# Kernel tuning notes

Hardware: AMD Instinct MI355X
Metric: run time of the kernel (lower is better)

## Reference

```python
import jax, jax.numpy as jnp
import numpy as np

N, L, D, H = 2, 2048, 1024, 16
DK = D // H  # 64


def setup_inputs() -> dict:
    key = jax.random.key(0)
    ks = jax.random.split(key, 8)
    Xq = jax.random.normal(ks[0], (N, L, D), dtype=jnp.float32)
    Xk = jax.random.normal(ks[1], (N, L, D), dtype=jnp.float32)
    Xv = jax.random.normal(ks[2], (N, L, D), dtype=jnp.float32)
    mask_2d = jax.random.randint(ks[3], (N, L, L), 0, 2, dtype=jnp.int32)
    scale = 0.02
    Wq = jax.random.normal(ks[4], (D, D), dtype=jnp.float32) * scale
    Wk = jax.random.normal(ks[5], (D, D), dtype=jnp.float32) * scale
    Wv = jax.random.normal(ks[6], (D, D), dtype=jnp.float32) * scale
    Wo = jax.random.normal(ks[7], (D, D), dtype=jnp.float32) * scale
    return {"Xq": Xq, "Xk": Xk, "Xv": Xv, "Wq": Wq, "Wk": Wk, "Wv": Wv, "Wo": Wo, "mask_2d": mask_2d}


def reference(Xq, Xk, Xv, Wq, Wk, Wv, Wo, mask_2d):
    # Projections (bias=False). Per-head slicing in the original == reshape to [N,L,H,DK].
    Q = (Xq @ Wq).reshape(N, L, H, DK)
    K = (Xk @ Wk).reshape(N, L, H, DK)
    V = (Xv @ Wv).reshape(N, L, H, DK)
    # Scaled dot-product scores: [N, H, L, L]
    scores = jnp.einsum("blhd,bmhd->bhlm", Q, K) / jnp.sqrt(jnp.asarray(DK, scores_dtype(Q)))
    # NOTE: original uses masked_fill(mask==0, 0) BEFORE softmax (zero-fill, not -inf).
    scores = jnp.where(mask_2d[:, None, :, :] == 0, jnp.zeros((), scores.dtype), scores)
    A = jax.nn.softmax(scores, axis=-1)
    O = jnp.einsum("bhlm,bmhd->blhd", A, V).reshape(N, L, D)
    return O @ Wo


def scores_dtype(Q):
    return Q.dtype
```

## Files before the change

### kernel.cpp

```cpp
#include <hip/hip_runtime.h>
#include <hip/hip_bf16.h>

#define NB 2
#define L_SEQ 2048
#define NH 16
#define DKH 64
#define DMODEL 1024
#define MROWS (NB * L_SEQ)
#define QSCALE 0.18033688f
#define DD (DMODEL * DMODEL)

typedef __attribute__((ext_vector_type(8))) short short8;
typedef __attribute__((ext_vector_type(4))) float f32x4;

static __device__ __forceinline__ unsigned short f2bf(float f) {
    unsigned u = __float_as_uint(f);
    u += 0x7fffu + ((u >> 16) & 1u);
    return (unsigned short)(u >> 16);
}

static __device__ __forceinline__ float fexp2(float x) {
#if __has_builtin(__builtin_amdgcn_exp2f)
    return __builtin_amdgcn_exp2f(x);
#else
    return __expf(x * 0.6931471806f);
#endif
}

static __device__ __forceinline__ unsigned pk_bf16(float a, float b) {
    __hip_bfloat162 h = __float22bfloat162_rn(make_float2(a, b));
    return *reinterpret_cast<unsigned*>(&h);
}

static __device__ __forceinline__ void gll16(const void* g, void* l) {
    __builtin_amdgcn_global_load_lds(
        (const __attribute__((address_space(1))) void*)g,
        (__attribute__((address_space(3))) void*)l, 16, 0, 0);
}

__global__ __launch_bounds__(256)
void prep(const float* __restrict__ Xq, const float* __restrict__ Xk,
          const float* __restrict__ Xv, const float* __restrict__ w0,
          const float* __restrict__ w1, const float* __restrict__ w2,
          const float* __restrict__ w3, const int* __restrict__ mask,
          unsigned short* __restrict__ XB, unsigned short* __restrict__ WtB,
          unsigned long long* __restrict__ MWT)
{
    __shared__ float ts[32][33];
    const int bx = blockIdx.x;
    const int t  = threadIdx.x;

    if (bx < 12288) {
        const int z = bx >> 12;
        const float* src = (z == 0) ? Xq : (z == 1) ? Xk : Xv;
        const size_t i4 = (size_t)(bx & 4095) * 256 + t;
        float4 v = ((const float4*)src)[i4];
        ushort4 o;
        o.x = f2bf(v.x); o.y = f2bf(v.y); o.z = f2bf(v.z); o.w = f2bf(v.w);
        ((ushort4*)(XB + (size_t)z * 4194304))[i4] = o;
    } else if (bx < 16384) {
        const int idx = bx - 12288;
        const int z   = idx >> 10;
        const int rem = idx & 1023;
        const float* W = (z == 0) ? w0 : (z == 1) ? w1 : (z == 2) ? w2 : w3;
        unsigned short* Wt = WtB + (size_t)z * DD;
        const int n0 = (rem & 31) * 32;
        const int k0 = (rem >> 5) * 32;
        const int r  = t >> 3;
        const int c  = (t & 7) * 4;
        float4 v = *(const float4*)&W[(size_t)(k0 + r) * DMODEL + n0 + c];
        ts[r][c + 0] = v.x; ts[r][c + 1] = v.y;
        ts[r][c + 2] = v.z; ts[r][c + 3] = v.w;
        __syncthreads();
        ushort4 o;
        o.x = f2bf(ts[c + 0][r]); o.y = f2bf(ts[c + 1][r]);
        o.z = f2bf(ts[c + 2][r]); o.w = f2bf(ts[c + 3][r]);
        *(ushort4*)&Wt[(size_t)(n0 + r) * DMODEL + k0 + c] = o;
    } else {
        const int lane = t & 63;
        const size_t wid = (size_t)(bx - 16384) * 4 + (t >> 6);
        const int mv = mask[wid * 64 + lane];
        const unsigned long long bits = __ballot(mv != 0);
        if (lane == 0) {
            const int b   = (int)(wid >> 16);
            const int rem = (int)(wid & 65535);
            const int row = rem >> 5;
            const int wd  = rem & 31;
            MWT[((size_t)b * 32 + wd) * L_SEQ + row] = bits;
        }
    }
}

__global__ __launch_bounds__(256)
void gemm_qkv(const unsigned short* __restrict__ XB,
              const unsigned short* __restrict__ WtB,
              unsigned short* __restrict__ QKV)
{
    __shared__ __align__(16) unsigned short SMEM[16384];

    const int t    = threadIdx.x;
    const int w    = t >> 6;
    const int lane = t & 63;
    const int z    = blockIdx.z;
    const int m0   = blockIdx.y * 128;
    const int n0   = blockIdx.x * 128;

    const unsigned short* A = XB  + (size_t)z * ((size_t)MROWS * DMODEL);
    const unsigned short* B = WtB + (size_t)z * DD;

    const int srow = lane >> 2;
    const int sc4  = (lane & 3) ^ (srow & 3);

    const unsigned short* ag[2];
    const unsigned short* bg[2];
    int lao[2], lbo[2];
#pragma unroll
    for (int g = 0; g < 2; ++g) {
        const int R = w * 32 + g * 16;
        ag[g] = A + (size_t)(m0 + R + srow) * DMODEL + sc4 * 8;
        bg[g] = B + (size_t)(n0 + R + srow) * DMODEL + sc4 * 8;
        lao[g] = R * 32;
        lbo[g] = R * 32;
    }

    const int ml = lane & 15;
    const int q  = lane >> 4;
    const int wm = (w >> 1) * 64;
    const int wn = (w & 1) * 64;

    const f32x4 z4 = {0.f, 0.f, 0.f, 0.f};
    f32x4 acc[4][4];
#pragma unroll
    for (int i = 0; i < 4; ++i)
#pragma unroll
        for (int j = 0; j < 4; ++j) acc[i][j] = z4;

#pragma unroll
    for (int g = 0; g < 2; ++g) {
        gll16(ag[g], &SMEM[lao[g]]);
        gll16(bg[g], &SMEM[8192 + lbo[g]]);
    }

    for (int j = 0; j < 32; ++j) {
        const int cur = j & 1;
        __syncthreads();
        if (j < 31) {
            const int kt = (j + 1) * 32;
            const int nb = (cur ^ 1) * 4096;
#pragma unroll
            for (int g = 0; g < 2; ++g) {
                gll16(ag[g] + kt, &SMEM[nb + lao[g]]);
                gll16(bg[g] + kt, &SMEM[8192 + nb + lbo[g]]);
            }
        }
        const unsigned short* As = &SMEM[cur * 4096];
        const unsigned short* Bs = &SMEM[8192 + cur * 4096];
        short8 av[4], bv[4];
#pragma unroll
        for (int mt = 0; mt < 4; ++mt)
            av[mt] = *(const short8*)
                &As[(wm + mt * 16 + ml) * 32 + ((q ^ (ml & 3)) * 8)];
#pragma unroll
        for (int nt = 0; nt < 4; ++nt)
            bv[nt] = *(const short8*)
                &Bs[(wn + nt * 16 + ml) * 32 + ((q ^ (ml & 3)) * 8)];
#pragma unroll
        for (int mt = 0; mt < 4; ++mt)
#pragma unroll
            for (int nt = 0; nt < 4; ++nt)
                acc[mt][nt] = __builtin_amdgcn_mfma_f32_16x16x32_bf16(
                    av[mt], bv[nt], acc[mt][nt], 0, 0, 0);
    }

    unsigned short* O = QKV + (size_t)z * ((size_t)MROWS * DMODEL);
    if (z == 2) {
        __syncthreads();
        unsigned short* Ts = SMEM;
#pragma unroll
        for (int mt = 0; mt < 4; ++mt) {
            const int trow0 = wm + mt * 16 + q * 4;
            const int ch    = trow0 >> 3;
#pragma unroll
            for (int nt = 0; nt < 4; ++nt) {
                const int tcol = wn + nt * 16 + ml;
                const int pc   = (ch & 8) | ((ch & 7) ^ (tcol & 7));
                ushort4 pv;
                pv.x = f2bf(acc[mt][nt][0]); pv.y = f2bf(acc[mt][nt][1]);
                pv.z = f2bf(acc[mt][nt][2]); pv.w = f2bf(acc[mt][nt][3]);
                *(ushort4*)&Ts[tcol * 128 + pc * 8 + (trow0 & 7)] = pv;
            }
        }
        __syncthreads();
        const int bb = m0 >> 11;
        const int l0 = (m0 & (L_SEQ - 1)) + (t & 15) * 8;
        const int cr = t & 15;
#pragma unroll
        for (int it = 0; it < 8; ++it) {
            const int tcol = (t >> 4) + 16 * it;
            const int pc   = (cr & 8) | ((cr & 7) ^ (tcol & 7));
            short8 vv = *(const short8*)&Ts[tcol * 128 + pc * 8];
            const int n  = n0 + tcol;
            const int hh = n >> 6;
            const int dk = n & (DKH - 1);
            *(short8*)&O[((size_t)(bb * NH + hh) * DKH + dk) * L_SEQ + l0] = vv;
        }
    } else {
        const float qs = (z == 0) ? QSCALE : 1.0f;
#pragma unroll
        for (int mt = 0; mt < 4; ++mt) {
            const int gr0 = m0 + wm + mt * 16 + q * 4;
#pragma unroll
            for (int nt = 0; nt < 4; ++nt) {
                const int col = n0 + wn + nt * 16 + ml;
                const int hh  = col >> 6;
                const int dk  = col & (DKH - 1);
#pragma unroll
                for (int r = 0; r < 4; ++r) {
                    const int row = gr0 + r;
                    const int bb  = row >> 11;
                    const int l   = row & (L_SEQ - 1);
                    O[(((size_t)(bb * NH + hh) * L_SEQ + l) << 6) + dk] =
                        f2bf(acc[mt][nt][r] * qs);
                }
            }
        }
    }
}

__global__ __launch_bounds__(256)
void gemm_out(const unsigned short* __restrict__ OB,
              const unsigned short* __restrict__ Wt,
              float* __restrict__ out)
{
    __shared__ __align__(16) unsigned short As[2][2048];
    __shared__ __align__(16) unsigned short Bs[2][4096];

    const int t    = threadIdx.x;
    const int w    = t >> 6;
    const int lane = t & 63;
    const int m0   = blockIdx.y * 64;
    const int n0   = blockIdx.x * 128;

    const int srow = lane >> 2;
    const int sc4  = (lane & 3) ^ (srow & 3);

    const unsigned short* ag =
        OB + (size_t)(m0 + w * 16 + srow) * DMODEL + sc4 * 8;
    const unsigned short* bg[2];
    int lbo[2];
#pragma unroll
    for (int g = 0; g < 2; ++g) {
        const int R = w * 32 + g * 16;
        bg[g] = Wt + (size_t)(n0 + R + srow) * DMODEL + sc4 * 8;
        lbo[g] = R * 32;
    }
    const int lao = (w * 16) * 32;

    const int ml = lane & 15;
    const int q  = lane >> 4;
    const int wm = (w >> 1) * 32;
    const int wn = (w & 1) * 64;

    const f32x4 z4 = {0.f, 0.f, 0.f, 0.f};
    f32x4 acc[2][4];
#pragma unroll
    for (int i = 0; i < 2; ++i)
#pragma unroll
        for (int j = 0; j < 4; ++j) acc[i][j] = z4;

    gll16(ag, &As[0][lao]);
#pragma unroll
    for (int g = 0; g < 2; ++g) gll16(bg[g], &Bs[0][lbo[g]]);

    for (int j = 0; j < 32; ++j) {
        const int cur = j & 1;
        __syncthreads();
        if (j < 31) {
            const int kt = (j + 1) * 32;
            gll16(ag + kt, &As[cur ^ 1][lao]);
#pragma unroll
            for (int g = 0; g < 2; ++g)
                gll16(bg[g] + kt, &Bs[cur ^ 1][lbo[g]]);
        }
        short8 av[2], bv[4];
#pragma unroll
        for (int mt = 0; mt < 2; ++mt)
            av[mt] = *(const short8*)
                &As[cur][(wm + mt * 16 + ml) * 32 + ((q ^ (ml & 3)) * 8)];
#pragma unroll
        for (int nt = 0; nt < 4; ++nt)
            bv[nt] = *(const short8*)
                &Bs[cur][(wn + nt * 16 + ml) * 32 + ((q ^ (ml & 3)) * 8)];
#pragma unroll
        for (int mt = 0; mt < 2; ++mt)
#pragma unroll
            for (int nt = 0; nt < 4; ++nt)
                acc[mt][nt] = __builtin_amdgcn_mfma_f32_16x16x32_bf16(
                    av[mt], bv[nt], acc[mt][nt], 0, 0, 0);
    }

#pragma unroll
    for (int mt = 0; mt < 2; ++mt) {
        const int gr0 = m0 + wm + mt * 16 + q * 4;
#pragma unroll
        for (int nt = 0; nt < 4; ++nt) {
            const int col = n0 + wn + nt * 16 + ml;
#pragma unroll
            for (int r = 0; r < 4; ++r)
                out[(size_t)(gr0 + r) * DMODEL + col] = acc[mt][nt][r];
        }
    }
}

__global__ __launch_bounds__(256, 4)
void attn_mfma(const unsigned short* __restrict__ Qb,
               const unsigned short* __restrict__ Kb,
               const unsigned short* __restrict__ Vtb,
               const unsigned long long* __restrict__ MWT,
               unsigned short* __restrict__ OB)
{
    __shared__ __align__(16) unsigned short Ks[2][4096];
    __shared__ __align__(16) unsigned short Vts[2][4096];
    __shared__ __align__(16) unsigned short Ps[4][1024];

    const int t    = threadIdx.x;
    const int w    = t >> 6;
    const int lane = t & 63;
    const int ml   = lane & 15;
    const int quad = lane >> 4;

    const int bid = blockIdx.x;
    const int p   = (bid >> 8) * 8 + (bid & 7);
    const int jq  = (bid >> 3) & 31;
    const int h   = p & 15;
    const int b   = p >> 4;
    const int q0  = jq * 64;

    const size_t hoff = (size_t)(b * NH + h) * L_SEQ * DKH;
    const unsigned short* Qh  = Qb  + hoff;
    const unsigned short* Kh  = Kb  + hoff;
    const unsigned short* Vth = Vtb + hoff;

    short8 qf[2];
#pragma unroll
    for (int s = 0; s < 2; ++s)
        qf[s] = *(const short8*)
            &Qh[(size_t)(q0 + w * 16 + ml) * DKH + (s * 4 + quad) * 8];

    const int srow = lane >> 3;
    const int sc   = (lane & 7) ^ srow;

    const unsigned short* kg0 = Kh + (size_t)(w * 16 + srow) * DKH + sc * 8;
    const unsigned short* kg1 = Kh + (size_t)(w * 16 + 8 + srow) * DKH + sc * 8;
    const unsigned short* vg0 = Vth + (size_t)(w * 16 + srow) * L_SEQ + sc * 8;
    const unsigned short* vg1 = Vth + (size_t)(w * 16 + 8 + srow) * L_SEQ + sc * 8;
    const int lk0 = (w * 16) * 64;
    const int lk1 = (w * 16 + 8) * 64;

    const unsigned long long* mg_w = MWT + (size_t)b * 32 * L_SEQ + q0 + w * 16;
    unsigned long long mcur = 0, mnxt = 0;
    if (lane < 16) mcur = mg_w[lane];

    f32x4 oacc[4];
    const f32x4 z4 = {0.f, 0.f, 0.f, 0.f};
#pragma unroll
    for (int dt = 0; dt < 4; ++dt) oacc[dt] = z4;
    float l_i = 0.f;

    gll16(kg0, &Ks[0][lk0]);  gll16(kg1, &Ks[0][lk1]);
    gll16(vg0, &Vts[0][lk0]); gll16(vg1, &Vts[0][lk1]);
    kg0 += 64 * DKH; kg1 += 64 * DKH; vg0 += 64; vg1 += 64;

    for (int j = 0; j < 32; ++j) {
        const int cur = j & 1;
        __syncthreads();
        if (j < 31) {
            const int nxt = cur ^ 1;
            gll16(kg0, &Ks[nxt][lk0]);  gll16(kg1, &Ks[nxt][lk1]);
            gll16(vg0, &Vts[nxt][lk0]); gll16(vg1, &Vts[nxt][lk1]);
            kg0 += 64 * DKH; kg1 += 64 * DKH; vg0 += 64; vg1 += 64;
            if (lane < 16) mnxt = mg_w[(size_t)(j + 1) * L_SEQ + lane];
        }

        f32x4 sacc[4];
#pragma unroll
        for (int kt = 0; kt < 4; ++kt) sacc[kt] = z4;
#pragma unroll
        for (int s = 0; s < 2; ++s) {
            short8 kf[4];
#pragma unroll
            for (int kt = 0; kt < 4; ++kt)
                kf[kt] = *(const short8*)
                    &Ks[cur][(kt * 16 + ml) * 64 + (((s * 4 + quad) ^ (ml & 7)) * 8)];
#pragma unroll
            for (int kt = 0; kt < 4; ++kt)
                sacc[kt] = __builtin_amdgcn_mfma_f32_16x16x32_bf16(
                    kf[kt], qf[s], sacc[kt], 0, 0, 0);
        }

        const unsigned long long wq = __shfl(mcur, ml) >> (quad * 4);
        const unsigned mlo = (unsigned)wq;
        const unsigned mhi = (unsigned)(wq >> 32);
        float rs = 0.f;
        float pr[4][4];
#pragma unroll
        for (int kt = 0; kt < 4; ++kt) {
            const unsigned word = (kt < 2) ? mlo : mhi;
            const int base = (kt & 1) * 16;
#pragma unroll
            for (int r = 0; r < 4; ++r) {
                const float mf = (float)((word >> (base + r)) & 1u);
                const float e  = fexp2(sacc[kt][r] * mf);
                pr[kt][r] = e;
                rs += e;
            }
        }
        rs += __shfl_xor(rs, 16);
        rs += __shfl_xor(rs, 32);
        l_i += rs;
#pragma unroll
        for (int kt = 0; kt < 4; ++kt) {
            uint2 pk;
            pk.x = pk_bf16(pr[kt][0], pr[kt][1]);
            pk.y = pk_bf16(pr[kt][2], pr[kt][3]);
            const int cp = (kt * 2 + (quad >> 1)) ^ (ml & 7);
            *(uint2*)&Ps[w][ml * 64 + cp * 8 + (quad & 1) * 4] = pk;
        }

#pragma unroll
        for (int s = 0; s < 2; ++s) {
            const short8 pf = *(const short8*)
                &Ps[w][ml * 64 + (((s * 4 + quad) ^ (ml & 7)) * 8)];
#pragma unroll
            for (int dt = 0; dt < 4; ++dt) {
                const short8 vf = *(const short8*)
                    &Vts[cur][(dt * 16 + ml) * 64 + (((s * 4 + quad) ^ (ml & 7)) * 8)];
                oacc[dt] = __builtin_amdgcn_mfma_f32_16x16x32_bf16(
                    vf, pf, oacc[dt], 0, 0, 0);
            }
        }
        mcur = mnxt;
    }

    const float inv = 1.0f / l_i;
    const int qrow = q0 + w * 16 + ml;
#pragma unroll
    for (int dt = 0; dt < 4; ++dt) {
        ushort4 o4;
        o4.x = f2bf(oacc[dt][0] * inv);
        o4.y = f2bf(oacc[dt][1] * inv);
        o4.z = f2bf(oacc[dt][2] * inv);
        o4.w = f2bf(oacc[dt][3] * inv);
        *(ushort4*)&OB[(size_t)(b * L_SEQ + qrow) * DMODEL + h * DKH +
                       dt * 16 + quad * 4] = o4;
    }
}

extern "C" void kernel_launch(void* const* d_in, const int* in_sizes, int n_in,
                              void* d_out, int out_size, void* d_ws, size_t ws_size,
                              hipStream_t stream)
{
    (void)in_sizes; (void)n_in; (void)out_size; (void)ws_size;

    const float* Xq   = (const float*)d_in[0];
    const float* Xk   = (const float*)d_in[1];
    const float* Xv   = (const float*)d_in[2];
    const float* Wq   = (const float*)d_in[3];
    const float* Wk   = (const float*)d_in[4];
    const float* Wv   = (const float*)d_in[5];
    const float* Wo   = (const float*)d_in[6];
    const int*   mask = (const int*)d_in[7];
    float* out = (float*)d_out;

    char* base = (char*)d_ws;
    unsigned short*     XB  = (unsigned short*)base;
    unsigned short*     WtB = (unsigned short*)(base + (24u << 20));
    unsigned short*     QKV = (unsigned short*)(base + (32u << 20));
    unsigned short*     OB  = (unsigned short*)(base + (56u << 20));
    unsigned long long* MWT = (unsigned long long*)(base + (64u << 20));

    const size_t tsz = (size_t)MROWS * DMODEL;

    prep<<<dim3(49152), 256, 0, stream>>>(
        Xq, Xk, Xv, Wq, Wk, Wv, Wo, mask, XB, WtB, MWT);

    gemm_qkv<<<dim3(8, 32, 3), 256, 0, stream>>>(XB, WtB, QKV);

    attn_mfma<<<dim3(1024), 256, 0, stream>>>(
        QKV, QKV + tsz, QKV + 2 * tsz, MWT, OB);

    gemm_out<<<dim3(8, 64), 256, 0, stream>>>(OB, WtB + 3 * (size_t)DD, out);
}
```

Baseline: 273.1 us.

## Remap GEMM blocks per XCD, stage QKV stores via LDS, single-buffer attention tiles

Both GEMMs now use a 1D grid whose block index is remapped so that neighbouring tiles land on the same XCD, aiming for better L2 reuse. The Q/K projection epilogue stages results through LDS so the head-major writes become 16-byte vector stores instead of scattered 2-byte stores. The attention kernel drops K/V double buffering for single buffers with two barriers per iteration, loads Q through LDS, and shares mask words via LDS instead of per-wave shuffles. That cuts LDS use, which may raise occupancy, but the loads for the next tile no longer overlap compute.

Measured after the change: 265.3 us. -2.9%, faster.

```diff
diff --git a/kernel.cpp b/kernel.cpp
--- a/kernel.cpp
+++ b/kernel.cpp
@@ -101,9 +101,14 @@
     const int t    = threadIdx.x;
     const int w    = t >> 6;
     const int lane = t & 63;
-    const int z    = blockIdx.z;
-    const int m0   = blockIdx.y * 128;
-    const int n0   = blockIdx.x * 128;
+
+    const int bid   = blockIdx.x;
+    const int xcd   = bid & 7;
+    const int idx   = bid >> 3;
+    const int pair  = xcd * 12 + (idx >> 3);
+    const int n0    = (idx & 7) * 128;
+    const int m0    = (pair & 31) * 128;
+    const int z     = pair >> 5;
 
     const unsigned short* A = XB  + (size_t)z * ((size_t)MROWS * DMODEL);
     const unsigned short* B = WtB + (size_t)z * DD;
@@ -173,9 +178,10 @@
     }
 
     unsigned short* O = QKV + (size_t)z * ((size_t)MROWS * DMODEL);
+    __syncthreads();
+    unsigned short* Ts = SMEM;
+
     if (z == 2) {
-        __syncthreads();
-        unsigned short* Ts = SMEM;
 #pragma unroll
         for (int mt = 0; mt < 4; ++mt) {
             const int trow0 = wm + mt * 16 + q * 4;
@@ -208,20 +214,32 @@
         const float qs = (z == 0) ? QSCALE : 1.0f;
 #pragma unroll
         for (int mt = 0; mt < 4; ++mt) {
-            const int gr0 = m0 + wm + mt * 16 + q * 4;
+            const int row0 = wm + mt * 16 + q * 4;
 #pragma unroll
             for (int nt = 0; nt < 4; ++nt) {
-                const int col = n0 + wn + nt * 16 + ml;
-                const int hh  = col >> 6;
-                const int dk  = col & (DKH - 1);
-#pragma unroll
-                for (int r = 0; r < 4; ++r) {
-                    const int row = gr0 + r;
-                    const int bb  = row >> 11;
-                    const int l   = row & (L_SEQ - 1);
-                    O[(((size_t)(bb * NH + hh) * L_SEQ + l) << 6) + dk] =
-                        f2bf(acc[mt][nt][r] * qs);
-                }
+                const int col = wn + nt * 16 + ml;
+#pragma unroll
+                for (int r = 0; r < 4; ++r)
+                    Ts[(row0 + r) * 128 + col] = f2bf(acc[mt][nt][r] * qs);
+            }
+        }
+        __syncthreads();
+        const int mloc = t >> 3;
+        const int c0   = t & 7;
+#pragma unroll
+        for (int pass = 0; pass < 4; ++pass) {
+#pragma unroll
+            for (int half = 0; half < 2; ++half) {
+                const int m = mloc + 32 * pass;
+                const int c = c0 + 8 * half;
+                short8 v = *(const short8*)&Ts[m * 128 + c * 8];
+                const int row = m0 + m;
+                const int bb  = row >> 11;
+                const int l   = row & (L_SEQ - 1);
+                const int n   = n0 + c * 8;
+                const int hh  = n >> 6;
+                const int dk  = n & (DKH - 1);
+                *(short8*)&O[(((size_t)(bb * NH + hh) * L_SEQ + l) << 6) + dk] = v;
             }
         }
     }
@@ -238,8 +256,12 @@
     const int t    = threadIdx.x;
     const int w    = t >> 6;
     const int lane = t & 63;
-    const int m0   = blockIdx.y * 64;
-    const int n0   = blockIdx.x * 128;
+
+    const int bid = blockIdx.x;
+    const int xcd = bid & 7;
+    const int idx = bid >> 3;
+    const int n0  = (idx & 7) * 128;
+    const int m0  = (xcd * 8 + (idx >> 3)) * 64;
 
     const int srow = lane >> 2;
     const int sc4  = (lane & 3) ^ (srow & 3);
@@ -319,9 +341,11 @@
                const unsigned long long* __restrict__ MWT,
                unsigned short* __restrict__ OB)
 {
-    __shared__ __align__(16) unsigned short Ks[2][4096];
-    __shared__ __align__(16) unsigned short Vts[2][4096];
-    __shared__ __align__(16) unsigned short Ps[4][1024];
+    __shared__ __align__(16) unsigned short Qs[64 * 64];
+    __shared__ __align__(16) unsigned short Ks[64 * 64];
+    __shared__ __align__(16) unsigned short Vts[64 * 64];
+    __shared__ __align__(16) unsigned short Ps[4][16 * 64];
+    __shared__ __align__(16) unsigned long long MskL[64];
 
     const int t    = threadIdx.x;
     const int w    = t >> 6;
@@ -341,25 +365,31 @@
     const unsigned short* Kh  = Kb  + hoff;
     const unsigned short* Vth = Vtb + hoff;
 
+    const int srow = lane >> 3;
+    const int sc   = (lane & 7) ^ srow;
+
+    gll16(Qh + (size_t)(q0 + w * 16 + srow) * DKH + sc * 8, &Qs[(w * 16) * 64]);
+    gll16(Qh + (size_t)(q0 + w * 16 + 8 + srow) * DKH + sc * 8, &Qs[(w * 16 + 8) * 64]);
+    __syncthreads();
+
     short8 qf[2];
 #pragma unroll
     for (int s = 0; s < 2; ++s)
         qf[s] = *(const short8*)
-            &Qh[(size_t)(q0 + w * 16 + ml) * DKH + (s * 4 + quad) * 8];
-
-    const int srow = lane >> 3;
-    const int sc   = (lane & 7) ^ srow;
+            &Qs[(w * 16 + ml) * 64 + (((s * 4 + quad) ^ (ml & 7)) * 8)];
 
     const unsigned short* kg0 = Kh + (size_t)(w * 16 + srow) * DKH + sc * 8;
     const unsigned short* kg1 = Kh + (size_t)(w * 16 + 8 + srow) * DKH + sc * 8;
     const unsigned short* vg0 = Vth + (size_t)(w * 16 + srow) * L_SEQ + sc * 8;
     const unsigned short* vg1 = Vth + (size_t)(w * 16 + 8 + srow) * L_SEQ + sc * 8;
-    const int lk0 = (w * 16) * 64;
-    const int lk1 = (w * 16 + 8) * 64;
-
-    const unsigned long long* mg_w = MWT + (size_t)b * 32 * L_SEQ + q0 + w * 16;
-    unsigned long long mcur = 0, mnxt = 0;
-    if (lane < 16) mcur = mg_w[lane];
+    unsigned short* lk0 = &Ks[(w * 16) * 64];
+    unsigned short* lk1 = &Ks[(w * 16 + 8) * 64];
+    unsigned short* lv0 = &Vts[(w * 16) * 64];
+    unsigned short* lv1 = &Vts[(w * 16 + 8) * 64];
+
+    const unsigned long long* mg = MWT + (size_t)b * 32 * L_SEQ + q0 + t;
+    unsigned long long m_pf = 0;
+    if (t < 64) m_pf = mg[0];
 
     f32x4 oacc[4];
     const f32x4 z4 = {0.f, 0.f, 0.f, 0.f};
@@ -367,20 +397,17 @@
     for (int dt = 0; dt < 4; ++dt) oacc[dt] = z4;
     float l_i = 0.f;
 
-    gll16(kg0, &Ks[0][lk0]);  gll16(kg1, &Ks[0][lk1]);
-    gll16(vg0, &Vts[0][lk0]); gll16(vg1, &Vts[0][lk1]);
-    kg0 += 64 * DKH; kg1 += 64 * DKH; vg0 += 64; vg1 += 64;
-
     for (int j = 0; j < 32; ++j) {
-        const int cur = j & 1;
-        __syncthreads();
-        if (j < 31) {
-            const int nxt = cur ^ 1;
-            gll16(kg0, &Ks[nxt][lk0]);  gll16(kg1, &Ks[nxt][lk1]);
-            gll16(vg0, &Vts[nxt][lk0]); gll16(vg1, &Vts[nxt][lk1]);
-            kg0 += 64 * DKH; kg1 += 64 * DKH; vg0 += 64; vg1 += 64;
-            if (lane < 16) mnxt = mg_w[(size_t)(j + 1) * L_SEQ + lane];
-        }
+        __syncthreads();
+        gll16(kg0, lk0);  gll16(kg1, lk1);
+        gll16(vg0, lv0);  gll16(vg1, lv1);
+        kg0 += 64 * DKH;  kg1 += 64 * DKH;
+        vg0 += 64;        vg1 += 64;
+        if (t < 64) {
+            MskL[t] = m_pf;
+            if (j < 31) m_pf = mg[(size_t)(j + 1) * L_SEQ];
+        }
+        __syncthreads();
 
         f32x4 sacc[4];
 #pragma unroll
@@ -391,14 +418,14 @@
 #pragma unroll
             for (int kt = 0; kt < 4; ++kt)
                 kf[kt] = *(const short8*)
-                    &Ks[cur][(kt * 16 + ml) * 64 + (((s * 4 + quad) ^ (ml & 7)) * 8)];
+                    &Ks[(kt * 16 + ml) * 64 + (((s * 4 + quad) ^ (ml & 7)) * 8)];
 #pragma unroll
             for (int kt = 0; kt < 4; ++kt)
                 sacc[kt] = __builtin_amdgcn_mfma_f32_16x16x32_bf16(
                     kf[kt], qf[s], sacc[kt], 0, 0, 0);
         }
 
-        const unsigned long long wq = __shfl(mcur, ml) >> (quad * 4);
+        const unsigned long long wq = MskL[w * 16 + ml] >> (quad * 4);
         const unsigned mlo = (unsigned)wq;
         const unsigned mhi = (unsigned)(wq >> 32);
         float rs = 0.f;
@@ -434,12 +461,11 @@
 #pragma unroll
             for (int dt = 0; dt < 4; ++dt) {
                 const short8 vf = *(const short8*)
-                    &Vts[cur][(dt * 16 + ml) * 64 + (((s * 4 + quad) ^ (ml & 7)) * 8)];
+                    &Vts[(dt * 16 + ml) * 64 + (((s * 4 + quad) ^ (ml & 7)) * 8)];
                 oacc[dt] = __builtin_amdgcn_mfma_f32_16x16x32_bf16(
                     vf, pf, oacc[dt], 0, 0, 0);
             }
         }
-        mcur = mnxt;
     }
 
     const float inv = 1.0f / l_i;
@@ -484,10 +510,10 @@
     prep<<<dim3(49152), 256, 0, stream>>>(
         Xq, Xk, Xv, Wq, Wk, Wv, Wo, mask, XB, WtB, MWT);
 
-    gemm_qkv<<<dim3(8, 32, 3), 256, 0, stream>>>(XB, WtB, QKV);
+    gemm_qkv<<<dim3(768), 256, 0, stream>>>(XB, WtB, QKV);
 
     attn_mfma<<<dim3(1024), 256, 0, stream>>>(
         QKV, QKV + tsz, QKV + 2 * tsz, MWT, OB);
 
-    gemm_out<<<dim3(8, 64), 256, 0, stream>>>(OB, WtB + 3 * (size_t)DD, out);
-}
+    gemm_out<<<dim3(512), 256, 0, stream>>>(OB, WtB + 3 * (size_t)DD, out);
+}
```
